# Kernel optimization log

Measured on AMD Instinct MI355X. Metric: run time of the kernel, lower is better.

## Reference

```python
import jax, jax.numpy as jnp
import numpy as np

B, S, D, H = 4, 2048, 1024, 16
DEPTH = D // H
NEG = -1e9


def setup_inputs() -> dict:
    key = jax.random.key(0)
    ks = jax.random.split(key, 10)
    scale = 1.0 / np.sqrt(D)
    return {
        "query": jax.random.normal(ks[0], (B, S, D), jnp.float32),
        "key": jax.random.normal(ks[1], (B, S, D), jnp.float32),
        "value": jax.random.normal(ks[2], (B, S, D), jnp.float32),
        "mask": jnp.zeros((B, 1, 1, S), jnp.float32),
        "Wq": jax.random.normal(ks[3], (D, D), jnp.float32) * scale,
        "bq": jnp.zeros((D,), jnp.float32),
        "Wk": jax.random.normal(ks[4], (D, D), jnp.float32) * scale,
        "bk": jnp.zeros((D,), jnp.float32),
        "Wv": jax.random.normal(ks[5], (D, D), jnp.float32) * scale,
        "bv": jnp.zeros((D,), jnp.float32),
        "Wo": jax.random.normal(ks[6], (D, D), jnp.float32) * scale,
        "bo": jnp.zeros((D,), jnp.float32),
    }


def _split_heads(x):
    # [B, S, D] -> [B, H, S, depth]
    b, s, _ = x.shape
    return x.reshape(b, s, H, DEPTH).transpose(0, 2, 1, 3)


def reference(query, key, value, mask, Wq, bq, Wk, bk, Wv, bv, Wo, bo):
    q = _split_heads(query @ Wq + bq)
    k = _split_heads(key @ Wk + bk)
    v = _split_heads(value @ Wv + bv)
    # scaled dot-product attention
    logits = jnp.einsum("bhqd,bhkd->bhqk", q, k) / jnp.sqrt(
        jnp.asarray(DEPTH, jnp.float32))
    logits = logits + mask * NEG
    attn = jax.nn.softmax(logits, axis=-1)
    out = jnp.einsum("bhqk,bhkd->bhqd", attn, v)
    # merge heads: [B,H,S,depth] -> [B,S,D]
    out = out.transpose(0, 2, 1, 3).reshape(query.shape[0], -1, D)
    out = out @ Wo + bo
    return out, attn
```

## Files before the change

kernel.cpp:

```cpp
#include <hip/hip_runtime.h>
#include <stdint.h>


typedef float f32x4 __attribute__((ext_vector_type(4)));
typedef __bf16 bf16x8 __attribute__((ext_vector_type(8)));
typedef unsigned short u16x4 __attribute__((ext_vector_type(4)));
typedef unsigned short u16x8 __attribute__((ext_vector_type(8)));

#define LOG2E 1.44269504088896340736f

static __device__ __forceinline__ f32x4 mfma16(bf16x8 a, bf16x8 b, f32x4 c) {
  return __builtin_amdgcn_mfma_f32_16x16x32_bf16(a, b, c, 0, 0, 0);
}
static __device__ __forceinline__ unsigned short bfc(float f) {
  return __builtin_bit_cast(unsigned short, (__bf16)f);
}
static __device__ __forceinline__ float e2(float x) { return __builtin_amdgcn_exp2f(x); }

#define GLDS16(g, l)                                                    \
  __builtin_amdgcn_global_load_lds(                                     \
      (const __attribute__((address_space(1))) void*)(g),               \
      (__attribute__((address_space(3))) void*)(l), 16, 0, 0)

struct Ptr3 { const float* s[3]; unsigned short* d[3]; };
struct Ptr4 { const float* s[4]; unsigned short* d[4]; };
struct QKArgs {
  const unsigned short* A[2];
  const unsigned short* Bt[2];
  const float* bias[2];
  unsigned short* C[2];
};

__global__ void cvt3(Ptr3 p) {
  const int z = blockIdx.z;
  const int i = (blockIdx.x * 256 + threadIdx.x) * 4;
  f32x4 v = *(const f32x4*)(const void*)(p.s[z] + i);
  u16x4 o;
  o[0] = bfc(v[0]); o[1] = bfc(v[1]); o[2] = bfc(v[2]); o[3] = bfc(v[3]);
  *(u16x4*)(void*)(p.d[z] + i) = o;
}

__global__ void wtrans4(Ptr4 p) {
  __shared__ float t[32][33];
  const int z = blockIdx.z;
  const float* W = p.s[z];
  unsigned short* Wt = p.d[z];
  const int tx = threadIdx.x & 31, ty = threadIdx.x >> 5;
  const int n0 = blockIdx.x * 32, k0 = blockIdx.y * 32;
#pragma unroll
  for (int i = 0; i < 4; ++i)
    t[ty + i * 8][tx] = W[(size_t)(k0 + ty + i * 8) * 1024 + n0 + tx];
  __syncthreads();
#pragma unroll
  for (int i = 0; i < 4; ++i)
    Wt[(size_t)(n0 + ty + i * 8) * 1024 + k0 + tx] = bfc(t[tx][ty + i * 8]);
}

#define GEMM_PROLOG(Aptr, Btptr)                                        \
  __shared__ unsigned short sA[128 * 32];                               \
  __shared__ unsigned short sB[128 * 32];                               \
  const int tid = threadIdx.x;                                          \
  const int m0 = blockIdx.x << 7, n0 = blockIdx.y << 7;                 \
  const int w = tid >> 6, lane = tid & 63, g = lane >> 4, r = lane & 15;\
  const int wr = w >> 1, wc = w & 1;                                    \
  const int srow = tid >> 2;                                            \
  const int scol = (tid & 3) << 3;                                      \
  const unsigned short* ga = (Aptr) + (size_t)(m0 + srow) * 1024 + scol;\
  const unsigned short* gb = (Btptr) + (size_t)(n0 + srow) * 1024 + scol;\
  unsigned short* la = sA + tid * 8;                                    \
  unsigned short* lb = sB + tid * 8;

#define GEMM_KLOOP(SWAP)                                                \
  for (int kt = 0; kt < 32; ++kt) {                                     \
    const int ko = kt << 5;                                             \
    GLDS16(ga + ko, la);                                                \
    GLDS16(ga + ko + 64 * 1024, la + 64 * 32);                          \
    GLDS16(gb + ko, lb);                                                \
    GLDS16(gb + ko + 64 * 1024, lb + 64 * 32);                          \
    __syncthreads();                                                    \
    bf16x8 af[4], bfv[4];                                               \
    _Pragma("unroll")                                                   \
    for (int i = 0; i < 4; ++i) {                                       \
      af[i]  = *(const bf16x8*)(const void*)&sA[(wr * 64 + i * 16 + r) * 32 + g * 8]; \
      bfv[i] = *(const bf16x8*)(const void*)&sB[(wc * 64 + i * 16 + r) * 32 + g * 8]; \
    }                                                                   \
    _Pragma("unroll")                                                   \
    for (int i = 0; i < 4; ++i)                                         \
      _Pragma("unroll")                                                 \
      for (int j = 0; j < 4; ++j)                                       \
        acc[i][j] = (SWAP) ? mfma16(bfv[j], af[i], acc[i][j])           \
                           : mfma16(af[i], bfv[j], acc[i][j]);          \
    __syncthreads();                                                    \
  }

__global__ __launch_bounds__(256, 2) void gemm_qk(QKArgs args) {
  const int z = blockIdx.z;
  const f32x4 fz = {0.f, 0.f, 0.f, 0.f};
  f32x4 acc[4][4];
#pragma unroll
  for (int i = 0; i < 4; ++i)
#pragma unroll
    for (int j = 0; j < 4; ++j) acc[i][j] = fz;
  GEMM_PROLOG(args.A[z], args.Bt[z])
  GEMM_KLOOP(1)
  const float osc = (z == 0) ? (0.125f * LOG2E) : 1.0f;
  unsigned short* Cq = args.C[z];
  const float* bias = args.bias[z];
#pragma unroll
  for (int j = 0; j < 4; ++j) {
    const int nb = n0 + wc * 64 + j * 16 + g * 4;
    const f32x4 b4 = *(const f32x4*)(const void*)(bias + nb);
#pragma unroll
    for (int i = 0; i < 4; ++i) {
      const int m = m0 + wr * 64 + i * 16 + r;
      const int bb = m >> 11, s = m & 2047, hh = nb >> 6, d = nb & 63;
      u16x4 pk;
#pragma unroll
      for (int t = 0; t < 4; ++t) pk[t] = bfc((acc[i][j][t] + b4[t]) * osc);
      *(u16x4*)(void*)(Cq + (size_t)(bb * 16 + hh) * 131072 + (size_t)s * 64 + d) = pk;
    }
  }
}

__global__ __launch_bounds__(256, 2) void gemm_v(const unsigned short* __restrict__ A,
                                                 const unsigned short* __restrict__ Bt,
                                                 const float* __restrict__ bias,
                                                 unsigned short* __restrict__ C) {
  const f32x4 fz = {0.f, 0.f, 0.f, 0.f};
  f32x4 acc[4][4];
#pragma unroll
  for (int i = 0; i < 4; ++i)
#pragma unroll
    for (int j = 0; j < 4; ++j) acc[i][j] = fz;
  GEMM_PROLOG(A, Bt)
  GEMM_KLOOP(0)
#pragma unroll
  for (int j = 0; j < 4; ++j) {
    const int n = n0 + wc * 64 + j * 16 + r;
    const float bv = bias[n];
    const int hh = n >> 6, d = n & 63;
#pragma unroll
    for (int i = 0; i < 4; ++i) {
      const int m = m0 + wr * 64 + i * 16 + g * 4;
      const int bb = m >> 11, s = m & 2047;
      u16x4 pk;
#pragma unroll
      for (int t = 0; t < 4; ++t) pk[t] = bfc(acc[i][j][t] + bv);
      *(u16x4*)(void*)(C + (size_t)(bb * 16 + hh) * 131072 + (size_t)d * 2048 + s) = pk;
    }
  }
}

__global__ __launch_bounds__(256, 2) void gemm_o(const unsigned short* __restrict__ A,
                                                 const unsigned short* __restrict__ Bt,
                                                 const float* __restrict__ bias,
                                                 float* __restrict__ C) {
  const f32x4 fz = {0.f, 0.f, 0.f, 0.f};
  f32x4 acc[4][4];
#pragma unroll
  for (int i = 0; i < 4; ++i)
#pragma unroll
    for (int j = 0; j < 4; ++j) acc[i][j] = fz;
  GEMM_PROLOG(A, Bt)
  GEMM_KLOOP(1)
#pragma unroll
  for (int j = 0; j < 4; ++j) {
    const int nb = n0 + wc * 64 + j * 16 + g * 4;
    const f32x4 b4 = *(const f32x4*)(const void*)(bias + nb);
#pragma unroll
    for (int i = 0; i < 4; ++i) {
      const int m = m0 + wr * 64 + i * 16 + r;
      f32x4 c;
#pragma unroll
      for (int t = 0; t < 4; ++t) c[t] = acc[i][j][t] + b4[t];
      *(f32x4*)(void*)(C + (size_t)m * 1024 + nb) = c;
    }
  }
}

#define LOADQF(dst, qrow0)                                                        \
  _Pragma("unroll")                                                               \
  for (int qc = 0; qc < 4; ++qc)                                                  \
    _Pragma("unroll")                                                             \
    for (int hf = 0; hf < 2; ++hf)                                                \
      dst[qc][hf] = *(const bf16x8*)(const void*)(Qb + (size_t)((qrow0) + qc * 16 + r) * 64 + hf * 32 + g * 8);

#define LOADKF(kf, kk)                                                            \
  _Pragma("unroll")                                                               \
  for (int ks = 0; ks < 2; ++ks)                                                  \
    _Pragma("unroll")                                                             \
    for (int hf = 0; hf < 2; ++hf)                                                \
      kf[ks][hf] = *(const bf16x8*)(const void*)(Kb + (size_t)((kk) + ks * 16 + r) * 64 + hf * 32 + g * 8);

#define LOADMP(mp0, mp1, kk)                                                      \
  {                                                                               \
    f32x4 mv0 = *(const f32x4*)(const void*)(mb + (kk) + g * 4);                  \
    f32x4 mv1 = *(const f32x4*)(const void*)(mb + (kk) + 16 + g * 4);             \
    _Pragma("unroll")                                                             \
    for (int j = 0; j < 4; ++j) { mp0[j] = mv0[j] * NEGM; mp1[j] = mv1[j] * NEGM; } \
  }

#define PASSA_CORE(qf, lreg, kf, mp0, mp1)                                        \
  _Pragma("unroll")                                                               \
  for (int qc = 0; qc < 4; ++qc) {                                                \
    f32x4 s0 = fz, s1 = fz;                                                       \
    s0 = mfma16(kf[0][0], qf[qc][0], s0);                                         \
    s0 = mfma16(kf[0][1], qf[qc][1], s0);                                         \
    s1 = mfma16(kf[1][0], qf[qc][0], s1);                                         \
    s1 = mfma16(kf[1][1], qf[qc][1], s1);                                         \
    float p = 0.f;                                                                \
    _Pragma("unroll")                                                             \
    for (int j = 0; j < 4; ++j) p += e2(s0[j] + mp0[j]) + e2(s1[j] + mp1[j]);     \
    lreg[qc] += p;                                                                \
  }

#define PASSB_CORE(qf, cL, oacc, kf, mp0, mp1, qrow, kk)                          \
  {                                                                               \
    _Pragma("unroll")                                                             \
    for (int ks = 0; ks < 2; ++ks) {                                              \
      _Pragma("unroll")                                                           \
      for (int qc = 0; qc < 4; ++qc) {                                            \
        f32x4 s = fz;                                                             \
        s = mfma16(kf[ks][0], qf[qc][0], s);                                      \
        s = mfma16(kf[ks][1], qf[qc][1], s);                                      \
        f32x4 pv;                                                                 \
        u16x4 pb;                                                                 \
        _Pragma("unroll")                                                         \
        for (int j = 0; j < 4; ++j) {                                             \
          const float val = e2(s[j] + (ks ? mp1[j] : mp0[j]) + cL[qc]);           \
          pv[j] = val;                                                            \
          pb[j] = bfc(val);                                                       \
        }                                                                         \
        __builtin_nontemporal_store(                                              \
            pv, (f32x4*)(void*)(ab + (size_t)((qrow) + qc * 16 + r) * 2048 + (kk) + ks * 16 + g * 4)); \
        *(u16x4*)(void*)(&Plds[w][(qc * 16 + r) * 40 + ks * 16 + g * 4]) = pb;    \
      }                                                                           \
    }                                                                             \
    bf16x8 vf[4];                                                                 \
    _Pragma("unroll")                                                             \
    for (int dn = 0; dn < 4; ++dn)                                                \
      vf[dn] = *(const bf16x8*)(const void*)(Vb + (size_t)(dn * 16 + r) * 2048 + (kk) + g * 8); \
    _Pragma("unroll")                                                             \
    for (int qs = 0; qs < 4; ++qs) {                                              \
      const bf16x8 pa = *(const bf16x8*)(const void*)(&Plds[w][(qs * 16 + r) * 40 + g * 8]); \
      _Pragma("unroll")                                                           \
      for (int dn = 0; dn < 4; ++dn) oacc[qs][dn] = mfma16(pa, vf[dn], oacc[qs][dn]); \
    }                                                                             \
  }

#define REDUCE_L(lreg)                                                            \
  _Pragma("unroll")                                                               \
  for (int qc = 0; qc < 4; ++qc) {                                                \
    lreg[qc] += __shfl_xor(lreg[qc], 16);                                         \
    lreg[qc] += __shfl_xor(lreg[qc], 32);                                         \
  }                                                                               \
  if (lane < 16) {                                                                \
    _Pragma("unroll")                                                             \
    for (int qc = 0; qc < 4; ++qc) sml[w][qc * 16 + lane] = lreg[qc];             \
  }

__global__ __launch_bounds__(256, 2) void attn_fused(const unsigned short* __restrict__ Qh,
                                                     const unsigned short* __restrict__ Kh,
                                                     const unsigned short* __restrict__ Vt,
                                                     const float* __restrict__ mask,
                                                     float* __restrict__ attn_out,
                                                     unsigned short* __restrict__ Obuf) {
  __shared__ unsigned short Plds[4][64 * 40];
  __shared__ float Osum[64][68];
  __shared__ float sml[4][64];

  const int blk = (blockIdx.x & 7) * 64 + (blockIdx.x >> 3);
  const int bh = blk >> 3;
  const int q0base = (blk & 7) << 8;
  const int b = bh >> 4, h = bh & 15;
  const int tid = threadIdx.x;
  const int w = tid >> 6, lane = tid & 63, g = lane >> 4, r = lane & 15;
  const float NEGM = -1e9f * LOG2E;

  const unsigned short* Qb = Qh + (size_t)bh * (2048 * 64);
  const unsigned short* Kb = Kh + (size_t)bh * (2048 * 64);
  const unsigned short* Vb = Vt + (size_t)bh * (64 * 2048);
  const float* mb = mask + (size_t)b * 2048;
  const f32x4 fz = {0.f, 0.f, 0.f, 0.f};
  float* ab = attn_out + (size_t)bh * 2048 * 2048;

  bf16x8 qfE[4][2], qfO[4][2];
  LOADQF(qfE, q0base)

  {
    float lreg0[4] = {0.f, 0.f, 0.f, 0.f};
    for (int step = 0; step < 16; ++step) {
      const int kk = (w << 9) + (step << 5);
      bf16x8 kf[2][2];
      LOADKF(kf, kk)
      f32x4 mp0, mp1;
      LOADMP(mp0, mp1, kk)
      PASSA_CORE(qfE, lreg0, kf, mp0, mp1)
    }
    REDUCE_L(lreg0)
  }
  __syncthreads();

#pragma unroll
  for (int t = 0; t < 4; ++t) {
    bf16x8(&qa)[4][2] = (t & 1) ? qfO : qfE;
    bf16x8(&qb)[4][2] = (t & 1) ? qfE : qfO;
    const int qrow = q0base + t * 64;

    float cL[4];
#pragma unroll
    for (int qc = 0; qc < 4; ++qc) {
      const int q = qc * 16 + r;
      cL[qc] = -__log2f(sml[0][q] + sml[1][q] + sml[2][q] + sml[3][q]);
    }

    f32x4 oacc[4][4];
#pragma unroll
    for (int i = 0; i < 4; ++i)
#pragma unroll
      for (int j = 0; j < 4; ++j) oacc[i][j] = fz;

    float lregB[4] = {0.f, 0.f, 0.f, 0.f};
    if (t < 3) { LOADQF(qb, qrow + 64) }

    for (int step = 0; step < 16; ++step) {
      const int kk = (w << 9) + (step << 5);
      bf16x8 kf[2][2];
      LOADKF(kf, kk)
      f32x4 mp0, mp1;
      LOADMP(mp0, mp1, kk)
      PASSB_CORE(qa, cL, oacc, kf, mp0, mp1, qrow, kk)
      if (t < 3) { PASSA_CORE(qb, lregB, kf, mp0, mp1) }
    }
    if (t < 3) { REDUCE_L(lregB) }

    for (int wv = 0; wv < 4; ++wv) {
      if (w == wv) {
#pragma unroll
        for (int qs = 0; qs < 4; ++qs)
#pragma unroll
          for (int dn = 0; dn < 4; ++dn)
#pragma unroll
            for (int j = 0; j < 4; ++j) {
              const int q = qs * 16 + g * 4 + j, d = dn * 16 + r;
              if (wv == 0) Osum[q][d] = oacc[qs][dn][j];
              else         Osum[q][d] += oacc[qs][dn][j];
            }
      }
      __syncthreads();
    }
    const int orow = tid >> 2, oc0 = (tid & 3) << 4;
#pragma unroll
    for (int half = 0; half < 2; ++half) {
      u16x8 pk;
#pragma unroll
      for (int j = 0; j < 8; ++j) pk[j] = bfc(Osum[orow][oc0 + half * 8 + j]);
      *(u16x8*)(void*)(Obuf + (size_t)(b * 2048 + qrow + orow) * 1024 + h * 64 + oc0 + half * 8) = pk;
    }
    __syncthreads();
  }
}

extern "C" void kernel_launch(void* const* d_in, const int* in_sizes, int n_in,
                              void* d_out, int out_size, void* d_ws, size_t ws_size,
                              hipStream_t stream) {
  const float* query = (const float*)d_in[0];
  const float* key_  = (const float*)d_in[1];
  const float* value = (const float*)d_in[2];
  const float* mask  = (const float*)d_in[3];
  const float* Wq = (const float*)d_in[4];
  const float* bq = (const float*)d_in[5];
  const float* Wk = (const float*)d_in[6];
  const float* bk = (const float*)d_in[7];
  const float* Wv = (const float*)d_in[8];
  const float* bv = (const float*)d_in[9];
  const float* Wo = (const float*)d_in[10];
  const float* bo = (const float*)d_in[11];

  uint8_t* ws = (uint8_t*)d_ws;
  unsigned short* XQ  = (unsigned short*)(ws);
  unsigned short* XK  = (unsigned short*)(ws + 16777216);
  unsigned short* XV  = (unsigned short*)(ws + 33554432);
  unsigned short* WTQ = (unsigned short*)(ws + 50331648);
  unsigned short* WTK = (unsigned short*)(ws + 52428800);
  unsigned short* WTV = (unsigned short*)(ws + 54525952);
  unsigned short* WTO = (unsigned short*)(ws + 56623104);
  unsigned short* QH  = (unsigned short*)(ws + 58720256);
  unsigned short* KH  = (unsigned short*)(ws + 75497472);
  unsigned short* VT  = (unsigned short*)(ws + 92274688);
  unsigned short* OB  = XQ;

  float* outp = (float*)d_out;
  float* attnp = outp + 8388608;

  Ptr3 pc = {{query, key_, value}, {XQ, XK, XV}};
  cvt3<<<dim3(8192, 1, 3), 256, 0, stream>>>(pc);
  Ptr4 pw = {{Wq, Wk, Wv, Wo}, {WTQ, WTK, WTV, WTO}};
  wtrans4<<<dim3(32, 32, 4), 256, 0, stream>>>(pw);
  QKArgs qk = {{XQ, XK}, {WTQ, WTK}, {bq, bk}, {QH, KH}};
  gemm_qk<<<dim3(64, 8, 2), 256, 0, stream>>>(qk);
  gemm_v<<<dim3(64, 8), 256, 0, stream>>>(XV, WTV, bv, VT);
  attn_fused<<<512, 256, 0, stream>>>(QH, KH, VT, mask, attnp, OB);
  gemm_o<<<dim3(64, 8), 256, 0, stream>>>(OB, WTO, bo, outp);
}
```

Baseline: 491.1 us.

## Stage bf16 probabilities in LDS and write attention rows coalesced

```diff
diff --git a/kernel.cpp b/kernel.cpp
--- a/kernel.cpp
+++ b/kernel.cpp
@@ -6,6 +6,7 @@
 typedef __bf16 bf16x8 __attribute__((ext_vector_type(8)));
 typedef unsigned short u16x4 __attribute__((ext_vector_type(4)));
 typedef unsigned short u16x8 __attribute__((ext_vector_type(8)));
+typedef unsigned int u32x2 __attribute__((ext_vector_type(2)));
 
 #define LOG2E 1.44269504088896340736f
 
@@ -16,6 +17,14 @@
   return __builtin_bit_cast(unsigned short, (__bf16)f);
 }
 static __device__ __forceinline__ float e2(float x) { return __builtin_amdgcn_exp2f(x); }
+static __device__ __forceinline__ float fb(unsigned int u) {
+  return __builtin_bit_cast(float, u);
+}
+#define BAR_LGKM()                                            \
+  do {                                                        \
+    asm volatile("s_waitcnt lgkmcnt(0)" ::: "memory");        \
+    __builtin_amdgcn_s_barrier();                             \
+  } while (0)
 
 #define GLDS16(g, l)                                                    \
   __builtin_amdgcn_global_load_lds(                                     \
@@ -214,40 +223,6 @@
     lreg[qc] += p;                                                                \
   }
 
-#define PASSB_CORE(qf, cL, oacc, kf, mp0, mp1, qrow, kk)                          \
-  {                                                                               \
-    _Pragma("unroll")                                                             \
-    for (int ks = 0; ks < 2; ++ks) {                                              \
-      _Pragma("unroll")                                                           \
-      for (int qc = 0; qc < 4; ++qc) {                                            \
-        f32x4 s = fz;                                                             \
-        s = mfma16(kf[ks][0], qf[qc][0], s);                                      \
-        s = mfma16(kf[ks][1], qf[qc][1], s);                                      \
-        f32x4 pv;                                                                 \
-        u16x4 pb;                                                                 \
-        _Pragma("unroll")                                                         \
-        for (int j = 0; j < 4; ++j) {                                             \
-          const float val = e2(s[j] + (ks ? mp1[j] : mp0[j]) + cL[qc]);           \
-          pv[j] = val;                                                            \
-          pb[j] = bfc(val);                                                       \
-        }                                                                         \
-        __builtin_nontemporal_store(                                              \
-            pv, (f32x4*)(void*)(ab + (size_t)((qrow) + qc * 16 + r) * 2048 + (kk) + ks * 16 + g * 4)); \
-        *(u16x4*)(void*)(&Plds[w][(qc * 16 + r) * 40 + ks * 16 + g * 4]) = pb;    \
-      }                                                                           \
-    }                                                                             \
-    bf16x8 vf[4];                                                                 \
-    _Pragma("unroll")                                                             \
-    for (int dn = 0; dn < 4; ++dn)                                                \
-      vf[dn] = *(const bf16x8*)(const void*)(Vb + (size_t)(dn * 16 + r) * 2048 + (kk) + g * 8); \
-    _Pragma("unroll")                                                             \
-    for (int qs = 0; qs < 4; ++qs) {                                              \
-      const bf16x8 pa = *(const bf16x8*)(const void*)(&Plds[w][(qs * 16 + r) * 40 + g * 8]); \
-      _Pragma("unroll")                                                           \
-      for (int dn = 0; dn < 4; ++dn) oacc[qs][dn] = mfma16(pa, vf[dn], oacc[qs][dn]); \
-    }                                                                             \
-  }
-
 #define REDUCE_L(lreg)                                                            \
   _Pragma("unroll")                                                               \
   for (int qc = 0; qc < 4; ++qc) {                                                \
@@ -265,8 +240,8 @@
                                                      const float* __restrict__ mask,
                                                      float* __restrict__ attn_out,
                                                      unsigned short* __restrict__ Obuf) {
-  __shared__ unsigned short Plds[4][64 * 40];
-  __shared__ float Osum[64][68];
+  constexpr int PITCH = 138;
+  __shared__ __align__(16) unsigned short PldsAll[4][64 * PITCH];
   __shared__ float sml[4][64];
 
   const int blk = (blockIdx.x & 7) * 64 + (blockIdx.x >> 3);
@@ -283,6 +258,9 @@
   const float* mb = mask + (size_t)b * 2048;
   const f32x4 fz = {0.f, 0.f, 0.f, 0.f};
   float* ab = attn_out + (size_t)bh * 2048 * 2048;
+  unsigned short* Pw = &PldsAll[w][0];
+  const int half = lane >> 5;
+  const int l5 = lane & 31;
 
   bf16x8 qfE[4][2], qfO[4][2];
   LOADQF(qfE, q0base)
@@ -299,13 +277,13 @@
     }
     REDUCE_L(lreg0)
   }
-  __syncthreads();
+  BAR_LGKM();
 
 #pragma unroll
   for (int t = 0; t < 4; ++t) {
     bf16x8(&qa)[4][2] = (t & 1) ? qfO : qfE;
     bf16x8(&qb)[4][2] = (t & 1) ? qfE : qfO;
-    const int qrow = q0base + t * 64;
+    const int q0 = q0base + t * 64;
 
     float cL[4];
 #pragma unroll
@@ -321,19 +299,61 @@
       for (int j = 0; j < 4; ++j) oacc[i][j] = fz;
 
     float lregB[4] = {0.f, 0.f, 0.f, 0.f};
-    if (t < 3) { LOADQF(qb, qrow + 64) }
-
-    for (int step = 0; step < 16; ++step) {
-      const int kk = (w << 9) + (step << 5);
-      bf16x8 kf[2][2];
-      LOADKF(kf, kk)
-      f32x4 mp0, mp1;
-      LOADMP(mp0, mp1, kk)
-      PASSB_CORE(qa, cL, oacc, kf, mp0, mp1, qrow, kk)
-      if (t < 3) { PASSA_CORE(qb, lregB, kf, mp0, mp1) }
+    if (t < 3) { LOADQF(qb, q0 + 64) }
+
+    for (int batch = 0; batch < 4; ++batch) {
+#pragma unroll
+      for (int sub = 0; sub < 4; ++sub) {
+        const int step = batch * 4 + sub;
+        const int kk = (w << 9) + (step << 5);
+        bf16x8 kf[2][2];
+        LOADKF(kf, kk)
+        f32x4 mp0, mp1;
+        LOADMP(mp0, mp1, kk)
+
+#pragma unroll
+        for (int ks = 0; ks < 2; ++ks) {
+#pragma unroll
+          for (int qc = 0; qc < 4; ++qc) {
+            f32x4 s = fz;
+            s = mfma16(kf[ks][0], qa[qc][0], s);
+            s = mfma16(kf[ks][1], qa[qc][1], s);
+            u16x4 pb;
+#pragma unroll
+            for (int j = 0; j < 4; ++j)
+              pb[j] = bfc(e2(s[j] + (ks ? mp1[j] : mp0[j]) + cL[qc]));
+            *(u16x4*)(void*)(&Pw[(qc * 16 + r) * PITCH + sub * 32 + ks * 16 + g * 4]) = pb;
+          }
+        }
+        bf16x8 vf[4];
+#pragma unroll
+        for (int dn = 0; dn < 4; ++dn)
+          vf[dn] = *(const bf16x8*)(const void*)(Vb + (size_t)(dn * 16 + r) * 2048 + kk + g * 8);
+#pragma unroll
+        for (int qs = 0; qs < 4; ++qs) {
+          const bf16x8 pa = *(const bf16x8*)(const void*)(&Pw[(qs * 16 + r) * PITCH + sub * 32 + g * 8]);
+#pragma unroll
+          for (int dn = 0; dn < 4; ++dn) oacc[qs][dn] = mfma16(pa, vf[dn], oacc[qs][dn]);
+        }
+        if (t < 3) { PASSA_CORE(qb, lregB, kf, mp0, mp1) }
+      }
+      const int colb = (w << 9) + (batch << 7);
+#pragma unroll 4
+      for (int i = 0; i < 32; ++i) {
+        const int row = i * 2 + half;
+        const u32x2 u = *(const u32x2*)(const void*)(&Pw[row * PITCH + l5 * 4]);
+        f32x4 o;
+        o[0] = fb(u[0] << 16);
+        o[1] = fb(u[0] & 0xFFFF0000u);
+        o[2] = fb(u[1] << 16);
+        o[3] = fb(u[1] & 0xFFFF0000u);
+        __builtin_nontemporal_store(
+            o, (f32x4*)(void*)(ab + (size_t)(q0 + row) * 2048 + colb + l5 * 4));
+      }
     }
     if (t < 3) { REDUCE_L(lregB) }
 
+    float (*Osum)[68] = reinterpret_cast<float (*)[68]>(&PldsAll[0][0]);
     for (int wv = 0; wv < 4; ++wv) {
       if (w == wv) {
 #pragma unroll
@@ -347,17 +367,17 @@
               else         Osum[q][d] += oacc[qs][dn][j];
             }
       }
-      __syncthreads();
+      BAR_LGKM();
     }
     const int orow = tid >> 2, oc0 = (tid & 3) << 4;
 #pragma unroll
-    for (int half = 0; half < 2; ++half) {
+    for (int hf2 = 0; hf2 < 2; ++hf2) {
       u16x8 pk;
 #pragma unroll
-      for (int j = 0; j < 8; ++j) pk[j] = bfc(Osum[orow][oc0 + half * 8 + j]);
-      *(u16x8*)(void*)(Obuf + (size_t)(b * 2048 + qrow + orow) * 1024 + h * 64 + oc0 + half * 8) = pk;
-    }
-    __syncthreads();
+      for (int j = 0; j < 8; ++j) pk[j] = bfc(Osum[orow][oc0 + hf2 * 8 + j]);
+      *(u16x8*)(void*)(Obuf + (size_t)(b * 2048 + q0 + orow) * 1024 + h * 64 + oc0 + hf2 * 8) = pk;
+    }
+    BAR_LGKM();
   }
 }
 
```

After: 595.6 us. 21.3% more time.
